# Kernel tuning notes

Hardware: AMD Instinct MI355X
Metric: run time of the kernel (lower is better)

The kernel has to match this reference:

```python
import jax, jax.numpy as jnp
import numpy as np
from jax import lax

SUB_NO = 20
T_NO = 401       # odd, so padding=T_NO//2 preserves length
N_E = 2000
N_I = 200
T_DATA = 50000
EXP_NO = 81
HID_NO = 6


def _conv1d(x, kern, pad, groups=1):
    # x: [N, C, L], kern: [O, I, K]; torch-style cross-correlation
    return lax.conv_general_dilated(
        x, kern, window_strides=(1,), padding=[(pad, pad)],
        dimension_numbers=('NCH', 'OIH', 'NCH'), feature_group_count=groups)


def setup_inputs() -> dict:
    key = jax.random.key(0)
    ks = jax.random.split(key, 8)
    rng = np.random.default_rng(0)

    # binary-tree dendrite: parent(j) = (j-1)//2; C_den[parent, child] = 1
    C_den = np.zeros((SUB_NO, SUB_NO), np.float32)
    for j in range(1, SUB_NO):
        C_den[(j - 1) // 2, j] = 1.0

    # one-hot synapse -> subunit assignment matrices
    C_syn_e = np.zeros((SUB_NO, N_E), np.float32)
    C_syn_e[rng.integers(0, SUB_NO, N_E), np.arange(N_E)] = 1.0
    C_syn_i = np.zeros((SUB_NO, N_I), np.float32)
    C_syn_i[rng.integers(0, SUB_NO, N_I), np.arange(N_I)] = 1.0

    # Gaussian-bump temporal basis (fixed buffer)
    raw = np.arange(T_NO, dtype=np.float32)
    points = np.arange(0, 5 * EXP_NO, 5, dtype=np.float32)
    exp_basis = np.exp(-(raw[None, :] - points[:, None]) ** 2 / 30.0).astype(np.float32)

    f32 = jnp.float32
    return {
        'S_e': jax.random.uniform(ks[0], (T_DATA, N_E), dtype=f32),
        'S_i': jax.random.uniform(ks[1], (T_DATA, N_I), dtype=f32),
        'Z': jax.random.bernoulli(ks[2], 0.02, (T_DATA,)).astype(f32),
        'W_syn': jax.random.normal(ks[3], (SUB_NO, 2), dtype=f32) * 0.01,
        'Tau_syn': jnp.ones((SUB_NO, 2), f32) * 3.0,
        'Delta_syn': jnp.ones((SUB_NO, 2), f32),
        'W_sub': jnp.ones((SUB_NO,), f32) * 0.1,
        'W_spk': jnp.ones((1,), f32),
        'Tau_spk': jnp.ones((1,), f32) * 3.0,
        'Theta': jnp.zeros((SUB_NO,), f32),
        'W_root_1': jax.random.normal(ks[4], (HID_NO, 1, EXP_NO), dtype=f32) * 0.01,
        'W_root_2': jax.random.normal(ks[5], (1, HID_NO, EXP_NO), dtype=f32) * 0.01,
        'C_den': jnp.asarray(C_den),
        'C_syn_e': jnp.asarray(C_syn_e),
        'C_syn_i': jnp.asarray(C_syn_i),
        'exp_basis': jnp.asarray(exp_basis),
    }


def reference(S_e, S_i, Z, W_syn, Tau_syn, Delta_syn, W_sub, W_spk, Tau_spk,
              Theta, W_root_1, W_root_2, C_den, C_syn_e, C_syn_i, exp_basis):
    T = S_e.shape[0]
    sub_no = C_den.shape[0]
    T_no = exp_basis.shape[1]

    # ---- spike_convolve ----
    syn_e = S_e @ C_syn_e.T          # [T, sub]
    syn_i = S_i @ C_syn_i.T          # [T, sub]

    t = jnp.arange(T_no, dtype=S_e.dtype)[None, :]            # [1, T_no]
    t_e = jnp.maximum(t - Delta_syn[:, 0:1], 0.0)
    t_i = jnp.maximum(t - Delta_syn[:, 1:2], 0.0)
    t_tau_e = t_e / Tau_syn[:, 0:1] ** 2
    t_tau_i = t_i / Tau_syn[:, 1:2] ** 2
    full_e_kern = t_tau_e * jnp.exp(-t_tau_e) * W_syn[:, 0:1] ** 2     # [sub, T_no]
    full_i_kern = -(t_tau_i * jnp.exp(-t_tau_i) * W_syn[:, 1:2] ** 2)  # [sub, T_no]

    ke = jnp.flip(full_e_kern, 1)[:, None, :]   # [sub, 1, T_no]
    ki = jnp.flip(full_i_kern, 1)[:, None, :]

    pad_e = jnp.pad(syn_e, ((T_no - 1, 0), (0, 0))).T[None]  # [1, sub, T+T_no-1]
    pad_i = jnp.pad(syn_i, ((T_no - 1, 0), (0, 0))).T[None]
    filt_e = _conv1d(pad_e, ke, 0, groups=sub_no)[0].T        # [T, sub]
    filt_i = _conv1d(pad_i, ki, 0, groups=sub_no)[0].T
    syn = filt_e + filt_i
    out_filters = jnp.concatenate([full_e_kern, full_i_kern], axis=0)  # [2*sub, T_no]

    # ---- subunit tree recursion (children have larger indices than parents) ----
    root_kern_1 = jnp.flip(jnp.matmul(W_root_1, exp_basis), 2)  # [hid, 1, T_no]
    root_kern_2 = jnp.flip(jnp.matmul(W_root_2, exp_basis), 2)  # [1, hid, T_no]
    w2 = W_sub ** 2

    ns_out = jnp.zeros((T, sub_no), S_e.dtype)
    for i in range(sub_no - 1, 0, -1):
        child = ns_out @ (C_den[i] * w2)                 # [T]
        ns_out = ns_out.at[:, i].set(jnp.tanh(syn[:, i] + Theta[i] + child))

    # root subunit with 2-layer temporal conv head
    child = ns_out @ (C_den[0] * w2)
    ns_in = syn[:, 0] + Theta[0] + child
    h = jnp.tanh(ns_in)[None, None, :]                   # [1, 1, T]
    h = jnp.tanh(_conv1d(h, root_kern_1, T_no // 2))     # [1, hid, T]
    final_Z = jax.nn.sigmoid(_conv1d(h, root_kern_2, T_no // 2).reshape(-1))  # [T]

    # ---- spike-history filter on Z ----
    t1 = jnp.arange(T_no, dtype=S_e.dtype)
    t_tau = t1 / Tau_spk ** 2
    spk_kern = jnp.flip(t_tau * jnp.exp(-t_tau) * W_spk ** 2, 0)[None, None, :]
    pad_Z = jnp.pad(Z, (T_no, 0))[None, None, :]         # [1, 1, T+T_no]
    final_V = _conv1d(pad_Z, spk_kern, 0).reshape(-1)[:-1]   # [T]

    return (final_V, final_Z, out_filters)
```

## Files before the change

kernel.cpp:

```cpp
#include <hip/hip_runtime.h>
#include <math.h>

#define T_DATA 50000
#define N_E 2000
#define N_I 200
#define SUB_NO 20
#define T_NO 401
#define KP 404
#define EXP_NO 81
#define HID_NO 6
#define ROWS 16

#define WS_SYN_ET   0
#define WS_SYN_IT   1000000
#define WS_SYNT     2000000
#define WS_H0       3000000
#define WS_H        3050000
#define WS_PART     3350000
#define WS_KE       3650000
#define WS_KI       3658080
#define WS_K1       3666160
#define WS_K2       3668584
#define WS_SPK      3671008
#define WS_ASGE     3671412
#define WS_ASGI     3671924

__global__ __launch_bounds__(256) void k_prep(
    const float* __restrict__ W_syn, const float* __restrict__ Tau_syn,
    const float* __restrict__ Delta_syn, const float* __restrict__ W_spk,
    const float* __restrict__ Tau_spk, const float* __restrict__ W_root_1,
    const float* __restrict__ W_root_2, const float* __restrict__ C_syn_e,
    const float* __restrict__ C_syn_i, const float* __restrict__ exp_basis,
    float* __restrict__ ws, unsigned int* __restrict__ asg_e,
    unsigned int* __restrict__ asg_i, float* __restrict__ out_filters) {
  const int bid = blockIdx.x, tid = threadIdx.x;
  if (bid == 0) {
    for (int u = tid; u < 512; u += 256) {
      unsigned int p = 0;
      for (int jj = 0; jj < 4; ++jj) {
        const int e = u * 4 + jj;
        int a = 20;
        if (e < N_E) {
          a = 0;
          for (int s = 0; s < SUB_NO; ++s) if (C_syn_e[s * N_E + e] > 0.5f) a = s;
        }
        p |= (unsigned int)a << (8 * jj);
      }
      asg_e[u] = p;
    }
  } else if (bid == 1) {
    for (int u = tid; u < 64; u += 256) {
      unsigned int p = 0;
      for (int jj = 0; jj < 4; ++jj) {
        const int e = u * 4 + jj;
        int a = 20;
        if (e < N_I) {
          a = 0;
          for (int s = 0; s < SUB_NO; ++s) if (C_syn_i[s * N_I + e] > 0.5f) a = s;
        }
        p |= (unsigned int)a << (8 * jj);
      }
      asg_i[u] = p;
    }
  } else if (bid == 2) {
    const float tau = Tau_spk[0], w = W_spk[0];
    const float it2 = 1.f / (tau * tau);
    for (int t = tid; t < KP; t += 256) {
      float v = 0.f;
      if (t < T_NO) { float tt = (float)t * it2; v = tt * __expf(-tt) * w * w; }
      ws[WS_SPK + t] = v;
    }
  } else if (bid < 3 + SUB_NO) {
    const int s = bid - 3;
    const float we = W_syn[s * 2], wi = W_syn[s * 2 + 1];
    const float te = Tau_syn[s * 2], ti = Tau_syn[s * 2 + 1];
    const float de = Delta_syn[s * 2], di = Delta_syn[s * 2 + 1];
    const float ie2 = 1.f / (te * te), ii2 = 1.f / (ti * ti);
    for (int t = tid; t < KP; t += 256) {
      float ve = 0.f, vi = 0.f;
      if (t < T_NO) {
        float xe = fmaxf((float)t - de, 0.f) * ie2;
        float xi = fmaxf((float)t - di, 0.f) * ii2;
        ve = xe * __expf(-xe) * we * we;
        vi = -(xi * __expf(-xi) * wi * wi);
        out_filters[s * T_NO + t] = ve;
        out_filters[(SUB_NO + s) * T_NO + t] = vi;
      }
      ws[WS_KE + s * KP + t] = ve;
      ws[WS_KI + s * KP + t] = vi;
    }
  } else {
    const int h = bid - (3 + SUB_NO);
    for (int t = tid; t < KP; t += 256) {
      float v1 = 0.f, v2 = 0.f;
      if (t < T_NO) {
        for (int b = 0; b < EXP_NO; ++b) {
          float bb = exp_basis[b * T_NO + t];
          v1 = fmaf(W_root_1[h * EXP_NO + b], bb, v1);
          v2 = fmaf(W_root_2[h * EXP_NO + b], bb, v2);
        }
      }
      ws[WS_K1 + h * KP + t] = v1;
      ws[WS_K2 + h * KP + t] = v2;
    }
  }
}

#define TSTR 260
__global__ __launch_bounds__(256) void k_seg(
    const float* __restrict__ S_e, const float* __restrict__ S_i,
    const unsigned int* __restrict__ asg_e, const unsigned int* __restrict__ asg_i,
    float* __restrict__ syn_eT, float* __restrict__ syn_iT) {
  __shared__ __align__(16) float tile[ROWS * TSTR];
  __shared__ float acc[256 * 21];
  __shared__ unsigned int asgl[512 + 64];
  const int tid = threadIdx.x;
  const int t0 = blockIdx.x * ROWS;
  const int r = tid & 15;
  const int sub = tid >> 4;
  float* __restrict__ myacc = acc + tid * 21;

  for (int i = tid; i < 512; i += 256) asgl[i] = asg_e[i];
  if (tid < 64) asgl[512 + tid] = asg_i[tid];
  #pragma unroll
  for (int i = 0; i < 21; ++i) myacc[i] = 0.f;
  __syncthreads();

  for (int ch = 0; ch < 8; ++ch) {
    #pragma unroll
    for (int i = 0; i < 4; ++i) {
      const int g = tid + i * 256;
      const int row = g >> 6, c4 = g & 63;
      const int col = ch * 256 + c4 * 4;
      float4 v = make_float4(0.f, 0.f, 0.f, 0.f);
      if (col < N_E) v = *(const float4*)(S_e + (size_t)(t0 + row) * N_E + col);
      *(float4*)(tile + row * TSTR + c4 * 4) = v;
    }
    __syncthreads();
    #pragma unroll
    for (int j = 0; j < 4; ++j) {
      const float4 v = *(const float4*)(tile + r * TSTR + sub * 16 + j * 4);
      const unsigned int a = asgl[ch * 64 + sub * 4 + j];
      myacc[a & 255] += v.x;
      myacc[(a >> 8) & 255] += v.y;
      myacc[(a >> 16) & 255] += v.z;
      myacc[a >> 24] += v.w;
    }
    __syncthreads();
  }
  for (int o = tid; o < ROWS * SUB_NO; o += 256) {
    const int row = o & 15, s = o >> 4;
    float sum = 0.f;
    #pragma unroll
    for (int c = 0; c < 16; ++c) sum += acc[(c * 16 + row) * 21 + s];
    syn_eT[s * T_DATA + t0 + row] = sum;
  }
  __syncthreads();
  #pragma unroll
  for (int i = 0; i < 21; ++i) myacc[i] = 0.f;

  #pragma unroll
  for (int i = 0; i < 4; ++i) {
    const int g = tid + i * 256;
    const int row = g >> 6, c4 = g & 63;
    const int col = c4 * 4;
    float4 v = make_float4(0.f, 0.f, 0.f, 0.f);
    if (col < N_I) v = *(const float4*)(S_i + (size_t)(t0 + row) * N_I + col);
    *(float4*)(tile + row * TSTR + c4 * 4) = v;
  }
  __syncthreads();
  #pragma unroll
  for (int j = 0; j < 4; ++j) {
    const float4 v = *(const float4*)(tile + r * TSTR + sub * 16 + j * 4);
    const unsigned int a = asgl[512 + sub * 4 + j];
    myacc[a & 255] += v.x;
    myacc[(a >> 8) & 255] += v.y;
    myacc[(a >> 16) & 255] += v.z;
    myacc[a >> 24] += v.w;
  }
  __syncthreads();
  for (int o = tid; o < ROWS * SUB_NO; o += 256) {
    const int row = o & 15, s = o >> 4;
    float sum = 0.f;
    #pragma unroll
    for (int c = 0; c < 16; ++c) sum += acc[(c * 16 + row) * 21 + s];
    syn_iT[s * T_DATA + t0 + row] = sum;
  }
}

template <int NOUT>
__device__ __forceinline__ void conv_acc(const float* __restrict__ xl,
                                         const float* __restrict__ kg,
                                         int lt, float* __restrict__ acc) {
  constexpr int NW = NOUT + 4;
  float xw[NW];
  #pragma unroll
  for (int r = 0; r < NW / 4; ++r) {
    float4 v = *(const float4*)(xl + lt + 400 + 4 * r);
    xw[4 * r + 0] = v.x; xw[4 * r + 1] = v.y;
    xw[4 * r + 2] = v.z; xw[4 * r + 3] = v.w;
  }
  const float* kp = kg;
  for (int g = 0; g < 100; ++g) {
    float4 kv = *(const float4*)kp; kp += 4;
    float kw[4] = {kv.x, kv.y, kv.z, kv.w};
    #pragma unroll
    for (int m = 0; m < 4; ++m)
      #pragma unroll
      for (int j = 0; j < NOUT; ++j)
        acc[j] = fmaf(kw[m], xw[4 + j - m], acc[j]);
    #pragma unroll
    for (int i = NW - 1; i >= 4; --i) xw[i] = xw[i - 4];
    float4 nv = *(const float4*)(xl + lt + 396 - 4 * g);
    xw[0] = nv.x; xw[1] = nv.y; xw[2] = nv.z; xw[3] = nv.w;
  }
  {
    float4 kv = *(const float4*)kp;
    float kw[4] = {kv.x, kv.y, kv.z, kv.w};
    #pragma unroll
    for (int m = 0; m < 4; ++m)
      #pragma unroll
      for (int j = 0; j < NOUT; ++j)
        acc[j] = fmaf(kw[m], xw[4 + j - m], acc[j]);
  }
}

__device__ __forceinline__ void fill_tile(float* __restrict__ xl,
                                          const float* __restrict__ X,
                                          int o, int n) {
  for (int i = threadIdx.x; i < n; i += blockDim.x) {
    int g = o + i;
    xl[i] = (g >= 0 && g < T_DATA) ? X[g] : 0.f;
  }
}

__global__ __launch_bounds__(256) void k_syn_conv(
    const float* __restrict__ syn_eT, const float* __restrict__ syn_iT,
    const float* __restrict__ ws, float* __restrict__ synT) {
  const int s = blockIdx.y;
  const int t0 = blockIdx.x * 2048;
  __shared__ __align__(16) float xe[2456];
  __shared__ __align__(16) float xi[2456];
  fill_tile(xe, syn_eT + s * T_DATA, t0 - 404, 2452);
  fill_tile(xi, syn_iT + s * T_DATA, t0 - 404, 2452);
  __syncthreads();
  const int lt = threadIdx.x * 8;
  float acc[8] = {0, 0, 0, 0, 0, 0, 0, 0};
  conv_acc<8>(xe, ws + WS_KE + s * KP, lt, acc);
  conv_acc<8>(xi, ws + WS_KI + s * KP, lt, acc);
  const int t = t0 + lt;
  #pragma unroll
  for (int j = 0; j < 8; ++j)
    if (t + j < T_DATA) synT[s * T_DATA + t + j] = acc[j];
}

__global__ __launch_bounds__(256) void k_tree(
    const float* __restrict__ synT, const float* __restrict__ Theta,
    const float* __restrict__ W_sub, float* __restrict__ h0) {
  const int t = blockIdx.x * 256 + threadIdx.x;
  if (t >= T_DATA) return;
  float ns[SUB_NO];
  #pragma unroll
  for (int i = SUB_NO - 1; i >= 1; --i) {
    float x = synT[i * T_DATA + t] + Theta[i];
    const int c1 = 2 * i + 1, c2 = 2 * i + 2;
    if (c1 < SUB_NO) { float w = W_sub[c1]; x = fmaf(w * w, ns[c1], x); }
    if (c2 < SUB_NO) { float w = W_sub[c2]; x = fmaf(w * w, ns[c2], x); }
    ns[i] = tanhf(x);
  }
  const float w1 = W_sub[1], w2 = W_sub[2];
  const float x0 = synT[t] + Theta[0] + w1 * w1 * ns[1] + w2 * w2 * ns[2];
  h0[t] = tanhf(x0);
}

__global__ __launch_bounds__(256) void k_root1(
    const float* __restrict__ h0, const float* __restrict__ ws,
    float* __restrict__ h_ws) {
  const int c = blockIdx.y;
  const int t0 = blockIdx.x * 1024;
  __shared__ __align__(16) float xt[1432];
  fill_tile(xt, h0, t0 + 200 - 404, 1428);
  __syncthreads();
  const int lt = threadIdx.x * 4;
  float acc[4] = {0, 0, 0, 0};
  conv_acc<4>(xt, ws + WS_K1 + c * KP, lt, acc);
  const int t = t0 + lt;
  #pragma unroll
  for (int j = 0; j < 4; ++j)
    if (t + j < T_DATA) h_ws[c * T_DATA + t + j] = tanhf(acc[j]);
}

__global__ __launch_bounds__(256) void k_root2(
    const float* __restrict__ h_ws, const float* __restrict__ ws,
    float* __restrict__ part) {
  const int c = blockIdx.y;
  const int t0 = blockIdx.x * 1024;
  __shared__ __align__(16) float xt[1432];
  fill_tile(xt, h_ws + c * T_DATA, t0 + 200 - 404, 1428);
  __syncthreads();
  const int lt = threadIdx.x * 4;
  float acc[4] = {0, 0, 0, 0};
  conv_acc<4>(xt, ws + WS_K2 + c * KP, lt, acc);
  const int t = t0 + lt;
  #pragma unroll
  for (int j = 0; j < 4; ++j)
    if (t + j < T_DATA) part[c * T_DATA + t + j] = acc[j];
}

__global__ __launch_bounds__(256) void k_comb(
    const float* __restrict__ part, float* __restrict__ outZ) {
  const int t = blockIdx.x * 256 + threadIdx.x;
  if (t >= T_DATA) return;
  float v = 0.f;
  #pragma unroll
  for (int c = 0; c < HID_NO; ++c) v += part[c * T_DATA + t];
  outZ[t] = 1.f / (1.f + __expf(-v));
}

__global__ __launch_bounds__(256) void k_spk(
    const float* __restrict__ Z, const float* __restrict__ ws,
    float* __restrict__ outV) {
  const int t0 = blockIdx.x * 1024;
  __shared__ __align__(16) float xt[1432];
  fill_tile(xt, Z, t0 - 1 - 404, 1428);
  __syncthreads();
  const int lt = threadIdx.x * 4;
  float acc[4] = {0, 0, 0, 0};
  conv_acc<4>(xt, ws + WS_SPK, lt, acc);
  const int t = t0 + lt;
  #pragma unroll
  for (int j = 0; j < 4; ++j)
    if (t + j < T_DATA) outV[t + j] = acc[j];
}

extern "C" void kernel_launch(void* const* d_in, const int* in_sizes, int n_in,
                              void* d_out, int out_size, void* d_ws, size_t ws_size,
                              hipStream_t stream) {
  const float* S_e      = (const float*)d_in[0];
  const float* S_i      = (const float*)d_in[1];
  const float* Z        = (const float*)d_in[2];
  const float* W_syn    = (const float*)d_in[3];
  const float* Tau_syn  = (const float*)d_in[4];
  const float* Delta_syn= (const float*)d_in[5];
  const float* W_sub    = (const float*)d_in[6];
  const float* W_spk    = (const float*)d_in[7];
  const float* Tau_spk  = (const float*)d_in[8];
  const float* Theta    = (const float*)d_in[9];
  const float* W_root_1 = (const float*)d_in[10];
  const float* W_root_2 = (const float*)d_in[11];
  const float* C_syn_e  = (const float*)d_in[13];
  const float* C_syn_i  = (const float*)d_in[14];
  const float* exp_basis= (const float*)d_in[15];

  float* ws = (float*)d_ws;
  unsigned int* asg_e = (unsigned int*)(ws + WS_ASGE);
  unsigned int* asg_i = (unsigned int*)(ws + WS_ASGI);
  float* out = (float*)d_out;

  k_prep<<<3 + SUB_NO + HID_NO, 256, 0, stream>>>(
      W_syn, Tau_syn, Delta_syn, W_spk, Tau_spk, W_root_1, W_root_2,
      C_syn_e, C_syn_i, exp_basis, ws, asg_e, asg_i, out + 2 * T_DATA);

  k_seg<<<T_DATA / ROWS, 256, 0, stream>>>(
      S_e, S_i, asg_e, asg_i, ws + WS_SYN_ET, ws + WS_SYN_IT);

  k_syn_conv<<<dim3(25, SUB_NO), 256, 0, stream>>>(
      ws + WS_SYN_ET, ws + WS_SYN_IT, ws, ws + WS_SYNT);

  k_tree<<<(T_DATA + 255) / 256, 256, 0, stream>>>(
      ws + WS_SYNT, Theta, W_sub, ws + WS_H0);

  k_root1<<<dim3(49, HID_NO), 256, 0, stream>>>(ws + WS_H0, ws, ws + WS_H);

  k_root2<<<dim3(49, HID_NO), 256, 0, stream>>>(ws + WS_H, ws, ws + WS_PART);

  k_comb<<<(T_DATA + 255) / 256, 256, 0, stream>>>(ws + WS_PART, out + T_DATA);

  k_spk<<<49, 256, 0, stream>>>(Z, ws, out);
}
```

Measured before the change: 191.5 us.

## Fuse tree into root conv, merge spike conv, use LDS atomics in segment sum

Rewrites the synapse segment-sum kernel to stream S_e/S_i rows directly and accumulate per-row subunit sums with LDS float atomics, dropping the staging tile and per-thread partial-sum reduction. Fuses the dendritic tree evaluation into the first root convolution's tile fill, which removes a kernel launch and the h0 round trip but recomputes the tree on halo positions for each of the six hidden channels. Merges the spike-history convolution into the second root-conv launch as an extra grid row. Replaces tanhf and the sigmoid division with exp/rcp approximations, trading some precision for fewer instructions.

```diff
diff --git a/kernel.cpp b/kernel.cpp
--- a/kernel.cpp
+++ b/kernel.cpp
@@ -14,16 +14,25 @@
 #define WS_SYN_ET   0
 #define WS_SYN_IT   1000000
 #define WS_SYNT     2000000
-#define WS_H0       3000000
-#define WS_H        3050000
-#define WS_PART     3350000
-#define WS_KE       3650000
-#define WS_KI       3658080
-#define WS_K1       3666160
-#define WS_K2       3668584
-#define WS_SPK      3671008
-#define WS_ASGE     3671412
-#define WS_ASGI     3671924
+#define WS_H        3000000
+#define WS_PART     3300000
+#define WS_KE       3600000
+#define WS_KI       3608080
+#define WS_K1       3616160
+#define WS_K2       3618584
+#define WS_SPK      3621008
+#define WS_ASGE     3621412
+#define WS_ASGI     3621924
+
+__device__ __forceinline__ float ftanh(float x) {
+  float e = __expf(2.f * x);
+  return 1.f - 2.f * __builtin_amdgcn_rcpf(e + 1.f);
+}
+
+__device__ __forceinline__ void ds_addf(float* p, float v) {
+  asm volatile("ds_add_f32 %0, %1"
+               :: "v"((unsigned int)(unsigned long long)p), "v"(v));
+}
 
 __global__ __launch_bounds__(256) void k_prep(
     const float* __restrict__ W_syn, const float* __restrict__ Tau_syn,
@@ -106,85 +115,63 @@
   }
 }
 
-#define TSTR 260
 __global__ __launch_bounds__(256) void k_seg(
     const float* __restrict__ S_e, const float* __restrict__ S_i,
     const unsigned int* __restrict__ asg_e, const unsigned int* __restrict__ asg_i,
     float* __restrict__ syn_eT, float* __restrict__ syn_iT) {
-  __shared__ __align__(16) float tile[ROWS * TSTR];
-  __shared__ float acc[256 * 21];
-  __shared__ unsigned int asgl[512 + 64];
+  __shared__ float accE[ROWS][21];
+  __shared__ float accI[ROWS][21];
+  __shared__ unsigned int asgl[576];
   const int tid = threadIdx.x;
   const int t0 = blockIdx.x * ROWS;
-  const int r = tid & 15;
-  const int sub = tid >> 4;
-  float* __restrict__ myacc = acc + tid * 21;
 
   for (int i = tid; i < 512; i += 256) asgl[i] = asg_e[i];
   if (tid < 64) asgl[512 + tid] = asg_i[tid];
-  #pragma unroll
-  for (int i = 0; i < 21; ++i) myacc[i] = 0.f;
+  for (int i = tid; i < ROWS * 21; i += 256) {
+    ((float*)accE)[i] = 0.f;
+    ((float*)accI)[i] = 0.f;
+  }
   __syncthreads();
 
-  for (int ch = 0; ch < 8; ++ch) {
-    #pragma unroll
-    for (int i = 0; i < 4; ++i) {
-      const int g = tid + i * 256;
+  {
+    const float* se = S_e + (size_t)t0 * N_E;
+    #pragma unroll 4
+    for (int k = 0; k < 32; ++k) {
+      const int g = tid + k * 256;
+      const int row = g >> 9, c4 = g & 511;
+      const int col = c4 * 4;
+      float4 v = make_float4(0.f, 0.f, 0.f, 0.f);
+      if (col < N_E) v = *(const float4*)(se + (size_t)row * N_E + col);
+      const unsigned int a = asgl[c4];
+      ds_addf(&accE[row][a & 255], v.x);
+      ds_addf(&accE[row][(a >> 8) & 255], v.y);
+      ds_addf(&accE[row][(a >> 16) & 255], v.z);
+      ds_addf(&accE[row][a >> 24], v.w);
+    }
+  }
+  {
+    const float* si = S_i + (size_t)t0 * N_I;
+    #pragma unroll
+    for (int k = 0; k < 4; ++k) {
+      const int g = tid + k * 256;
       const int row = g >> 6, c4 = g & 63;
-      const int col = ch * 256 + c4 * 4;
+      const int col = c4 * 4;
       float4 v = make_float4(0.f, 0.f, 0.f, 0.f);
-      if (col < N_E) v = *(const float4*)(S_e + (size_t)(t0 + row) * N_E + col);
-      *(float4*)(tile + row * TSTR + c4 * 4) = v;
-    }
-    __syncthreads();
-    #pragma unroll
-    for (int j = 0; j < 4; ++j) {
-      const float4 v = *(const float4*)(tile + r * TSTR + sub * 16 + j * 4);
-      const unsigned int a = asgl[ch * 64 + sub * 4 + j];
-      myacc[a & 255] += v.x;
-      myacc[(a >> 8) & 255] += v.y;
-      myacc[(a >> 16) & 255] += v.z;
-      myacc[a >> 24] += v.w;
-    }
-    __syncthreads();
-  }
+      if (col < N_I) v = *(const float4*)(si + (size_t)row * N_I + col);
+      const unsigned int a = asgl[512 + c4];
+      ds_addf(&accI[row][a & 255], v.x);
+      ds_addf(&accI[row][(a >> 8) & 255], v.y);
+      ds_addf(&accI[row][(a >> 16) & 255], v.z);
+      ds_addf(&accI[row][a >> 24], v.w);
+    }
+  }
+  asm volatile("s_waitcnt lgkmcnt(0)" ::: "memory");
+  __syncthreads();
+
   for (int o = tid; o < ROWS * SUB_NO; o += 256) {
     const int row = o & 15, s = o >> 4;
-    float sum = 0.f;
-    #pragma unroll
-    for (int c = 0; c < 16; ++c) sum += acc[(c * 16 + row) * 21 + s];
-    syn_eT[s * T_DATA + t0 + row] = sum;
-  }
-  __syncthreads();
-  #pragma unroll
-  for (int i = 0; i < 21; ++i) myacc[i] = 0.f;
-
-  #pragma unroll
-  for (int i = 0; i < 4; ++i) {
-    const int g = tid + i * 256;
-    const int row = g >> 6, c4 = g & 63;
-    const int col = c4 * 4;
-    float4 v = make_float4(0.f, 0.f, 0.f, 0.f);
-    if (col < N_I) v = *(const float4*)(S_i + (size_t)(t0 + row) * N_I + col);
-    *(float4*)(tile + row * TSTR + c4 * 4) = v;
-  }
-  __syncthreads();
-  #pragma unroll
-  for (int j = 0; j < 4; ++j) {
-    const float4 v = *(const float4*)(tile + r * TSTR + sub * 16 + j * 4);
-    const unsigned int a = asgl[512 + sub * 4 + j];
-    myacc[a & 255] += v.x;
-    myacc[(a >> 8) & 255] += v.y;
-    myacc[(a >> 16) & 255] += v.z;
-    myacc[a >> 24] += v.w;
-  }
-  __syncthreads();
-  for (int o = tid; o < ROWS * SUB_NO; o += 256) {
-    const int row = o & 15, s = o >> 4;
-    float sum = 0.f;
-    #pragma unroll
-    for (int c = 0; c < 16; ++c) sum += acc[(c * 16 + row) * 21 + s];
-    syn_iT[s * T_DATA + t0 + row] = sum;
+    syn_eT[s * T_DATA + t0 + row] = accE[row][s];
+    syn_iT[s * T_DATA + t0 + row] = accI[row][s];
   }
 }
 
@@ -254,32 +241,32 @@
     if (t + j < T_DATA) synT[s * T_DATA + t + j] = acc[j];
 }
 
-__global__ __launch_bounds__(256) void k_tree(
+__global__ __launch_bounds__(256) void k_root1tree(
     const float* __restrict__ synT, const float* __restrict__ Theta,
-    const float* __restrict__ W_sub, float* __restrict__ h0) {
-  const int t = blockIdx.x * 256 + threadIdx.x;
-  if (t >= T_DATA) return;
-  float ns[SUB_NO];
-  #pragma unroll
-  for (int i = SUB_NO - 1; i >= 1; --i) {
-    float x = synT[i * T_DATA + t] + Theta[i];
-    const int c1 = 2 * i + 1, c2 = 2 * i + 2;
-    if (c1 < SUB_NO) { float w = W_sub[c1]; x = fmaf(w * w, ns[c1], x); }
-    if (c2 < SUB_NO) { float w = W_sub[c2]; x = fmaf(w * w, ns[c2], x); }
-    ns[i] = tanhf(x);
-  }
-  const float w1 = W_sub[1], w2 = W_sub[2];
-  const float x0 = synT[t] + Theta[0] + w1 * w1 * ns[1] + w2 * w2 * ns[2];
-  h0[t] = tanhf(x0);
-}
-
-__global__ __launch_bounds__(256) void k_root1(
-    const float* __restrict__ h0, const float* __restrict__ ws,
+    const float* __restrict__ W_sub, const float* __restrict__ ws,
     float* __restrict__ h_ws) {
   const int c = blockIdx.y;
   const int t0 = blockIdx.x * 1024;
   __shared__ __align__(16) float xt[1432];
-  fill_tile(xt, h0, t0 + 200 - 404, 1428);
+  const int o = t0 + 200 - 404;
+  for (int i = threadIdx.x; i < 1428; i += 256) {
+    const int t = o + i;
+    float h = 0.f;
+    if (t >= 0 && t < T_DATA) {
+      float ns[SUB_NO];
+      #pragma unroll
+      for (int q = SUB_NO - 1; q >= 1; --q) {
+        float x = synT[q * T_DATA + t] + Theta[q];
+        const int c1 = 2 * q + 1, c2 = 2 * q + 2;
+        if (c1 < SUB_NO) { float w = W_sub[c1]; x = fmaf(w * w, ns[c1], x); }
+        if (c2 < SUB_NO) { float w = W_sub[c2]; x = fmaf(w * w, ns[c2], x); }
+        ns[q] = ftanh(x);
+      }
+      const float w1 = W_sub[1], w2 = W_sub[2];
+      h = ftanh(synT[t] + Theta[0] + w1 * w1 * ns[1] + w2 * w2 * ns[2]);
+    }
+    xt[i] = h;
+  }
   __syncthreads();
   const int lt = threadIdx.x * 4;
   float acc[4] = {0, 0, 0, 0};
@@ -287,24 +274,35 @@
   const int t = t0 + lt;
   #pragma unroll
   for (int j = 0; j < 4; ++j)
-    if (t + j < T_DATA) h_ws[c * T_DATA + t + j] = tanhf(acc[j]);
-}
-
-__global__ __launch_bounds__(256) void k_root2(
-    const float* __restrict__ h_ws, const float* __restrict__ ws,
-    float* __restrict__ part) {
+    if (t + j < T_DATA) h_ws[c * T_DATA + t + j] = ftanh(acc[j]);
+}
+
+__global__ __launch_bounds__(256) void k_root2spk(
+    const float* __restrict__ h_ws, const float* __restrict__ Z,
+    const float* __restrict__ ws, float* __restrict__ part,
+    float* __restrict__ outV) {
   const int c = blockIdx.y;
   const int t0 = blockIdx.x * 1024;
   __shared__ __align__(16) float xt[1432];
-  fill_tile(xt, h_ws + c * T_DATA, t0 + 200 - 404, 1428);
-  __syncthreads();
   const int lt = threadIdx.x * 4;
   float acc[4] = {0, 0, 0, 0};
-  conv_acc<4>(xt, ws + WS_K2 + c * KP, lt, acc);
-  const int t = t0 + lt;
-  #pragma unroll
-  for (int j = 0; j < 4; ++j)
-    if (t + j < T_DATA) part[c * T_DATA + t + j] = acc[j];
+  if (c < HID_NO) {
+    fill_tile(xt, h_ws + c * T_DATA, t0 + 200 - 404, 1428);
+    __syncthreads();
+    conv_acc<4>(xt, ws + WS_K2 + c * KP, lt, acc);
+    const int t = t0 + lt;
+    #pragma unroll
+    for (int j = 0; j < 4; ++j)
+      if (t + j < T_DATA) part[c * T_DATA + t + j] = acc[j];
+  } else {
+    fill_tile(xt, Z, t0 - 1 - 404, 1428);
+    __syncthreads();
+    conv_acc<4>(xt, ws + WS_SPK, lt, acc);
+    const int t = t0 + lt;
+    #pragma unroll
+    for (int j = 0; j < 4; ++j)
+      if (t + j < T_DATA) outV[t + j] = acc[j];
+  }
 }
 
 __global__ __launch_bounds__(256) void k_comb(
@@ -314,23 +312,7 @@
   float v = 0.f;
   #pragma unroll
   for (int c = 0; c < HID_NO; ++c) v += part[c * T_DATA + t];
-  outZ[t] = 1.f / (1.f + __expf(-v));
-}
-
-__global__ __launch_bounds__(256) void k_spk(
-    const float* __restrict__ Z, const float* __restrict__ ws,
-    float* __restrict__ outV) {
-  const int t0 = blockIdx.x * 1024;
-  __shared__ __align__(16) float xt[1432];
-  fill_tile(xt, Z, t0 - 1 - 404, 1428);
-  __syncthreads();
-  const int lt = threadIdx.x * 4;
-  float acc[4] = {0, 0, 0, 0};
-  conv_acc<4>(xt, ws + WS_SPK, lt, acc);
-  const int t = t0 + lt;
-  #pragma unroll
-  for (int j = 0; j < 4; ++j)
-    if (t + j < T_DATA) outV[t + j] = acc[j];
+  outZ[t] = __builtin_amdgcn_rcpf(1.f + __expf(-v));
 }
 
 extern "C" void kernel_launch(void* const* d_in, const int* in_sizes, int n_in,
@@ -367,14 +349,11 @@
   k_syn_conv<<<dim3(25, SUB_NO), 256, 0, stream>>>(
       ws + WS_SYN_ET, ws + WS_SYN_IT, ws, ws + WS_SYNT);
 
-  k_tree<<<(T_DATA + 255) / 256, 256, 0, stream>>>(
-      ws + WS_SYNT, Theta, W_sub, ws + WS_H0);
-
-  k_root1<<<dim3(49, HID_NO), 256, 0, stream>>>(ws + WS_H0, ws, ws + WS_H);
-
-  k_root2<<<dim3(49, HID_NO), 256, 0, stream>>>(ws + WS_H, ws, ws + WS_PART);
+  k_root1tree<<<dim3(49, HID_NO), 256, 0, stream>>>(
+      ws + WS_SYNT, Theta, W_sub, ws, ws + WS_H);
+
+  k_root2spk<<<dim3(49, HID_NO + 1), 256, 0, stream>>>(
+      ws + WS_H, Z, ws, ws + WS_PART, out);
 
   k_comb<<<(T_DATA + 255) / 256, 256, 0, stream>>>(ws + WS_PART, out + T_DATA);
-
-  k_spk<<<49, 256, 0, stream>>>(Z, ws, out);
-}
+}
```

New measurement: 716.6 us. 3.74x slower.
